# Performance work log

Hardware: AMD Instinct MI355X
Metric: run time of the kernel (lower is better)

## Reference

```python
import jax, jax.numpy as jnp
import numpy as np

N_AQI, N_MEO = 35, 18
N = N_AQI + N_MEO
F_OUT = 64
CTX = 60
D = F_OUT + CTX            # per-node feature dim inside pairwise concat
ALPHA = 0.2                # leakyrelu negative slope
B = 4096
IN_AQI, IN_MEO = 16, 16
NEG = -1e12


def _xavier(key, shape):
    fan_in, fan_out = shape[0], shape[-1]
    gain = 1.414
    bound = gain * np.sqrt(6.0 / (fan_in + fan_out))
    return jax.random.uniform(key, shape, jnp.float32, -bound, bound)


def setup_inputs() -> dict:
    key = jax.random.key(0)
    ks = jax.random.split(key, 32)
    inp = {
        "aqi_inp": jax.random.normal(ks[0], (B, N_AQI, IN_AQI), jnp.float32),
        "meo_inp": jax.random.normal(ks[1], (B, N_MEO, IN_MEO), jnp.float32),
        "context_feat": jax.random.normal(ks[2], (N, CTX), jnp.float32),
        "adj_norm": jax.random.uniform(ks[3], (N, N), jnp.float32),
        # embedding tables (all 2-dim embeddings as in the module)
        "aqi_idE": jax.random.normal(ks[4], (35, 2), jnp.float32),
        "aqi_monthE": jax.random.normal(ks[5], (13, 2), jnp.float32),
        "aqi_weekdayE": jax.random.normal(ks[6], (7, 2), jnp.float32),
        "aqi_hourE": jax.random.normal(ks[7], (24, 2), jnp.float32),
        "meo_windE": jax.random.normal(ks[8], (9, 2), jnp.float32),
        "meo_idE": jax.random.normal(ks[9], (18, 2), jnp.float32),
        "meo_monthE": jax.random.normal(ks[10], (13, 2), jnp.float32),
        "meo_weekdayE": jax.random.normal(ks[11], (7, 2), jnp.float32),
        "meo_hourE": jax.random.normal(ks[12], (24, 2), jnp.float32),
        # projection weights
        "W_xa": _xavier(ks[13], (IN_AQI, F_OUT)),
        "W_xm": _xavier(ks[14], (IN_MEO, F_OUT)),
        "W_ua": _xavier(ks[15], (IN_AQI + 8, F_OUT)),
        "W_um": _xavier(ks[16], (IN_MEO + 10, F_OUT)),
        # attention vectors: 2*F_OUT + 121 = 2*D + 1
        "a_aa": _xavier(ks[17], (2 * F_OUT + 121, 1)),
        "a_am": _xavier(ks[18], (2 * F_OUT + 121, 1)),
        "a_ma": _xavier(ks[19], (2 * F_OUT + 121, 1)),
        "a_mm": _xavier(ks[20], (2 * F_OUT + 121, 1)),
        # integer inputs
        "aqi_ex": jax.random.randint(ks[21], (B, N_AQI, 4), 0, 7, jnp.int32),
        "meo_ex": jax.random.randint(ks[22], (B, N_MEO, 5), 0, 7, jnp.int32),
        "adj": jax.random.randint(ks[23], (N, N), 0, 2, jnp.int32),
    }
    return inp


def _block(hf_src, hf_dst, an_block, a):
    # e[b,i,j] = leakyrelu(hf_src[b,i].a_src + hf_dst[b,j].a_dst + an[i,j]*a_last)
    d = hf_src.shape[-1]
    s = hf_src @ a[:d, 0]                        # [B, Ns]
    t = hf_dst @ a[d:2 * d, 0]                   # [B, Nd]
    e = s[:, :, None] + t[:, None, :] + an_block * a[2 * d, 0]
    return jax.nn.leaky_relu(e, ALPHA)


def reference(aqi_inp, meo_inp, context_feat, adj_norm,
              aqi_idE, aqi_monthE, aqi_weekdayE, aqi_hourE,
              meo_windE, meo_idE, meo_monthE, meo_weekdayE, meo_hourE,
              W_xa, W_xm, W_ua, W_um, a_aa, a_am, a_ma, a_mm,
              aqi_ex, meo_ex, adj):
    # value projection (pre-embedding features)
    attri_aqi = aqi_inp @ W_xa                   # [B, 35, F]
    attri_meo = meo_inp @ W_xm                   # [B, 18, F]
    heter_attri = jnp.concatenate([attri_aqi, attri_meo], axis=1)  # [B, 53, F]

    # append external-feature embeddings
    aqi_full = jnp.concatenate([
        aqi_inp, aqi_idE[aqi_ex[:, :, 0]], aqi_monthE[aqi_ex[:, :, 1]],
        aqi_weekdayE[aqi_ex[:, :, 2]], aqi_hourE[aqi_ex[:, :, 3]]], axis=2)
    meo_full = jnp.concatenate([
        meo_inp, meo_windE[meo_ex[:, :, 0]], meo_idE[meo_ex[:, :, 1]],
        meo_monthE[meo_ex[:, :, 2]], meo_weekdayE[meo_ex[:, :, 3]],
        meo_hourE[meo_ex[:, :, 4]]], axis=2)

    heter_aqi = aqi_full @ W_ua                  # [B, 35, F]
    heter_meo = meo_full @ W_um                  # [B, 18, F]
    hf = jnp.concatenate([heter_aqi, heter_meo], axis=1)            # [B, 53, F]
    ctx = jnp.broadcast_to(context_feat[None], (hf.shape[0], N, CTX))
    hf = jnp.concatenate([hf, ctx], axis=2)      # [B, 53, D]

    # pairwise scores per heterogeneous sub-block (decomposed, no N*N*D tensor)
    hfa, hfm = hf[:, :N_AQI], hf[:, N_AQI:]
    e_aa = _block(hfa, hfa, adj_norm[:N_AQI, :N_AQI], a_aa)
    e_am = _block(hfa, hfm, adj_norm[:N_AQI, N_AQI:], a_am)
    e_ma = _block(hfm, hfa, adj_norm[N_AQI:, :N_AQI], a_ma)
    e_mm = _block(hfm, hfm, adj_norm[N_AQI:, N_AQI:], a_mm)
    e = jnp.concatenate([
        jnp.concatenate([e_aa, e_am], axis=2),
        jnp.concatenate([e_ma, e_mm], axis=2)], axis=1)             # [B, 53, 53]

    attention = jax.nn.softmax(jnp.where(adj[None] > 0, e, NEG), axis=2)
    heter_out = attention @ heter_attri          # [B, 53, F]
    return heter_out[:, :N_AQI, :], heter_out[:, N_AQI:, :]
```

## Files before the change

### kernel.cpp

```cpp
#include <hip/hip_runtime.h>
#include <hip/hip_bf16.h>

#define NAQ 35
#define NME 18
#define NN  53
#define FD  64
#define CTXD 60
#define PERB 2

#define CVI_F   1024
#define CVE_F   1152
#define SVC_F   1248
#define EBW_F   1460
#define WS_FLOATS 4428

#define L_CVI   0
#define L_CVE   128
#define L_SVC   224
#define L_AF    436
#define L_EFA   1716
#define L_EFM   2031
#define L_SVW   2229
#define L_PT    2444
#define L_ATT   4748
#define S_TOTAL 7052
#define P_STR   72
#define AF_STR  40

typedef unsigned int   u32;
typedef unsigned short u16;
typedef short s8v __attribute__((ext_vector_type(8)));
typedef float f4v __attribute__((ext_vector_type(4)));

__device__ __forceinline__ float ldf(const void* p, long i, bool bf) {
  if (bf) { u16 h = ((const u16*)p)[i]; return __uint_as_float(((u32)h) << 16); }
  return ((const float*)p)[i];
}
__device__ __forceinline__ u16 f2bf(float f) {
  u32 u = __float_as_uint(f);
  return (u16)((u + 0x7FFFu + ((u >> 16) & 1u)) >> 16);
}
__device__ __forceinline__ bool sniff_bf16(const void* ctx) {
  const u32* w = (const u32*)ctx;
  bool ok = true;
#pragma unroll
  for (int k = 0; k < 32; ++k) {
    u32 e = (w[k] >> 7) & 0xFFu;
    ok = ok && (e >= 96u && e <= 160u);
  }
  return ok;
}
__device__ __forceinline__ s8v ld_frag(const u16* p) {
  union { float4 f; s8v s; } u;
  u.f = *(const float4*)(const void*)p;
  return u.s;
}

__global__ void prep_kernel(
    const void* __restrict__ ctx, const void* __restrict__ adjn,
    const void* __restrict__ Wxa, const void* __restrict__ Wxm,
    const void* __restrict__ Wua, const void* __restrict__ Wum,
    const void* __restrict__ a_aa, const void* __restrict__ a_am,
    const void* __restrict__ a_ma, const void* __restrict__ a_mm,
    const int* __restrict__ adj, float* __restrict__ ws)
{
  const bool bf = sniff_bf16(ctx);
  int tid = blockIdx.x * blockDim.x + threadIdx.x;
  if (tid < 2048) {
    int n = tid >> 5, kk = tid & 31;
    float v = (kk < 16) ? ldf(Wxa, kk * 64 + n, bf)
                        : ldf(Wxm, (kk - 16) * 64 + n, bf);
    ((u16*)ws)[tid] = f2bf(v);
    return;
  }
  int fi = tid - 1024;
  if (fi < CVE_F) {
    int idx = fi - CVI_F;
    int tr = idx >> 4, k = idx & 15;
    const void* Wu = (tr < 4) ? Wua : Wum;
    const void* av; int off;
    switch (tr) {
      case 0: av = a_aa; off = 0;   break;
      case 1: av = a_am; off = 0;   break;
      case 2: av = a_aa; off = 124; break;
      case 3: av = a_ma; off = 124; break;
      case 4: av = a_ma; off = 0;   break;
      case 5: av = a_mm; off = 0;   break;
      case 6: av = a_am; off = 124; break;
      default: av = a_mm; off = 124; break;
    }
    float s = 0.f;
    for (int f = 0; f < 64; ++f) s += ldf(Wu, k * 64 + f, bf) * ldf(av, off + f, bf);
    ws[fi] = s;
  } else if (fi < SVC_F) {
    int idx = fi - CVE_F;
    int tr = idx / 12, e = idx - tr * 12;
    int E = (tr < 4) ? 8 : 10;
    float v = 0.f;
    if (e < E) {
      const void* Wu = (tr < 4) ? Wua : Wum;
      const void* av; int off;
      switch (tr) {
        case 0: av = a_aa; off = 0;   break;
        case 1: av = a_am; off = 0;   break;
        case 2: av = a_aa; off = 124; break;
        case 3: av = a_ma; off = 124; break;
        case 4: av = a_ma; off = 0;   break;
        case 5: av = a_mm; off = 0;   break;
        case 6: av = a_am; off = 124; break;
        default: av = a_mm; off = 124; break;
      }
      float s = 0.f;
      for (int f = 0; f < 64; ++f) s += ldf(Wu, (16 + e) * 64 + f, bf) * ldf(av, off + f, bf);
      v = s;
    }
    ws[fi] = v;
  } else if (fi < EBW_F) {
    int idx = fi - SVC_F;
    int arr = idx / 53, i = idx - arr * 53;
    int isA = (i < NAQ);
    const void* av; int off;
    if (arr == 0)      { av = isA ? a_aa : a_ma; off = 64;  }
    else if (arr == 1) { av = isA ? a_am : a_mm; off = 64;  }
    else if (arr == 2) { av = isA ? a_aa : a_am; off = 188; }
    else               { av = isA ? a_ma : a_mm; off = 188; }
    float s = 0.f;
    for (int c = 0; c < CTXD; ++c) s += ldf(ctx, i * CTXD + c, bf) * ldf(av, off + c, bf);
    ws[fi] = s;
  } else if (fi < WS_FLOATS) {
    int idx = fi - EBW_F;
    int i = idx / 56, j = idx - i * 56;
    float v = 1e30f;
    if (j < NN && adj[i * NN + j] > 0) {
      const void* aq = (i < NAQ) ? ((j < NAQ) ? a_aa : a_am)
                                 : ((j < NAQ) ? a_ma : a_mm);
      v = ldf(adjn, i * NN + j, bf) * ldf(aq, 248, bf);
    }
    ws[fi] = v;
  }
}

__global__ __launch_bounds__(256, 5) void hga_main(
    const void* __restrict__ aqi_inp, const void* __restrict__ meo_inp,
    const void* __restrict__ ctx,
    const void* __restrict__ aqi_idE, const void* __restrict__ aqi_monthE,
    const void* __restrict__ aqi_weekdayE, const void* __restrict__ aqi_hourE,
    const void* __restrict__ meo_windE, const void* __restrict__ meo_idE,
    const void* __restrict__ meo_monthE, const void* __restrict__ meo_weekdayE,
    const void* __restrict__ meo_hourE,
    const int* __restrict__ aqi_ex, const int* __restrict__ meo_ex,
    const float* __restrict__ ws, void* __restrict__ out, int B)
{
  __shared__ __align__(16) float sm[S_TOTAL];
  const int t = threadIdx.x;
  const bool bf = sniff_bf16(ctx);
  u16* AFu = (u16*)(sm + L_AF);
  u16* ATu = (u16*)(sm + L_ATT);
  u16* Pu  = (u16*)(sm + L_PT);

  {
    const float4* src = (const float4*)(ws + CVI_F);
    float4* dst = (float4*)sm;
    for (int v = t; v < 109; v += 256) dst[v] = src[v];
  }
  __syncthreads();

  for (int e = 0; e < PERB; ++e) {
    const int b = blockIdx.x * PERB + e;
    if (b >= B) break;

    for (int idx = t; idx < 654; idx += 256) {
      if (idx < 140) {
        int r = idx >> 2, j = idx & 3;
        uint2 v;
        if (bf) v = ((const uint2*)aqi_inp)[((long)b * NAQ + r) * 4 + j];
        else {
          float4 f = ((const float4*)aqi_inp)[((long)b * NAQ + r) * 4 + j];
          v.x = ((u32)f2bf(f.y) << 16) | f2bf(f.x);
          v.y = ((u32)f2bf(f.w) << 16) | f2bf(f.z);
        }
        *(uint2*)(AFu + r * AF_STR + j * 4) = v;
      } else if (idx < 212) {
        int z = idx - 140;
        int i = z >> 2, j = z & 3;
        uint2 v;
        if (bf) v = ((const uint2*)meo_inp)[((long)b * NME + i) * 4 + j];
        else {
          float4 f = ((const float4*)meo_inp)[((long)b * NME + i) * 4 + j];
          v.x = ((u32)f2bf(f.y) << 16) | f2bf(f.x);
          v.y = ((u32)f2bf(f.w) << 16) | f2bf(f.z);
        }
        *(uint2*)(AFu + (NAQ + i) * AF_STR + 16 + j * 4) = v;
      } else if (idx < 352) {
        int z = idx - 212;
        int r = z >> 2, j = z & 3;
        *(uint2*)(AFu + r * AF_STR + 16 + j * 4) = make_uint2(0, 0);
      } else if (idx < 424) {
        int z = idx - 352;
        int i = z >> 2, j = z & 3;
        *(uint2*)(AFu + (NAQ + i) * AF_STR + j * 4) = make_uint2(0, 0);
      } else if (idx < 564) {
        int z = idx - 424;
        int r = z >> 2, p = z & 3;
        int ee = aqi_ex[((long)b * NAQ + r) * 4 + p];
        const void* tbl = (p == 0) ? aqi_idE : (p == 1) ? aqi_monthE
                         : (p == 2) ? aqi_weekdayE : aqi_hourE;
        sm[L_EFA + r * 9 + p * 2]     = ldf(tbl, ee * 2, bf);
        sm[L_EFA + r * 9 + p * 2 + 1] = ldf(tbl, ee * 2 + 1, bf);
      } else {
        int z = idx - 564;
        int i = z / 5, p = z - i * 5;
        int ee = meo_ex[((long)b * NME + i) * 5 + p];
        const void* tbl = (p == 0) ? meo_windE : (p == 1) ? meo_idE
                         : (p == 2) ? meo_monthE : (p == 3) ? meo_weekdayE : meo_hourE;
        sm[L_EFM + i * 11 + p * 2]     = ldf(tbl, ee * 2, bf);
        sm[L_EFM + i * 11 + p * 2 + 1] = ldf(tbl, ee * 2 + 1, bf);
      }
    }
    {
      int c = t & 63;
      for (int kk = t >> 6; kk < 11; kk += 4) ATu[c * P_STR + 53 + kk] = 0;
    }
    __syncthreads();

    {
      const int lane = t & 63, w = t >> 6;
      const int mm = lane & 15, q4 = lane >> 4;
      s8v av = ld_frag(AFu + (16 * w + mm) * AF_STR + q4 * 8);
      const u16* wt = (const u16*)ws;
      s8v bv0 = ld_frag(wt + (mm)      * 32 + q4 * 8);
      s8v bv1 = ld_frag(wt + (16 + mm) * 32 + q4 * 8);
      s8v bv2 = ld_frag(wt + (32 + mm) * 32 + q4 * 8);
      s8v bv3 = ld_frag(wt + (48 + mm) * 32 + q4 * 8);
#pragma unroll
      for (int nt = 0; nt < 4; ++nt) {
        f4v acc = {0.f, 0.f, 0.f, 0.f};
        s8v bv = (nt == 0) ? bv0 : (nt == 1) ? bv1 : (nt == 2) ? bv2 : bv3;
        acc = __builtin_amdgcn_mfma_f32_16x16x32_bf16(av, bv, acc, 0, 0, 0);
        const int c = nt * 16 + mm;
#pragma unroll
        for (int reg = 0; reg < 4; ++reg) {
          const int r = 16 * w + q4 * 4 + reg;
          if (r < NN) ATu[c * P_STR + r] = f2bf(acc[reg]);
        }
      }
      if (t < 212) {
        const int r = t >> 2, role = t & 3;
        const bool isA = (r < NAQ);
        const int tr = (isA ? 0 : 4) + role;
        const u16* arow = AFu + r * AF_STR + (isA ? 0 : 16);
        const float* Ci = sm + L_CVI + tr * 16;
        float s = 0.f;
#pragma unroll
        for (int k = 0; k < 16; ++k)
          s = fmaf(__uint_as_float(((u32)arow[k]) << 16), Ci[k], s);
        const int E = isA ? 8 : 10;
        const float* Ef = isA ? (sm + L_EFA + r * 9) : (sm + L_EFM + (r - NAQ) * 11);
        const float* Ce = sm + L_CVE + tr * 12;
        for (int k = 0; k < E; ++k) s = fmaf(Ef[k], Ce[k], s);
        sm[L_SVW + role * 53 + r] = sm[L_SVC + role * 53 + r] + s;
      }
    }
    __syncthreads();

    {
      const int r = t >> 2, q = t & 3;
      const int j0 = q * 14;
      if (r < NN) {
        float ev[14];
        float m = -3.0e38f, ssum = 0.f;
        const float s1 = sm[L_SVW + r], s2 = sm[L_SVW + 53 + r];
        const float* tb = sm + L_SVW + ((r < NAQ) ? 106 : 159);
        const float* ebrow = ws + EBW_F + r * 56;
#pragma unroll
        for (int jj = 0; jj < 14; ++jj) {
          const int j = j0 + jj;
          float v = -3.0e38f;
          if (j < NN) {
            float eb = ebrow[j];
            float rr = ((j < NAQ) ? s1 : s2) + tb[j] + eb;
            v = (eb > 1e29f) ? -1.0e12f : ((rr > 0.f) ? rr : 0.2f * rr);
          }
          ev[jj] = v;
          m = fmaxf(m, v);
        }
        m = fmaxf(m, __shfl_xor(m, 1, 64));
        m = fmaxf(m, __shfl_xor(m, 2, 64));
#pragma unroll
        for (int jj = 0; jj < 14; ++jj) {
          float pv = ((j0 + jj) < NN) ? __expf(ev[jj] - m) : 0.f;
          ev[jj] = pv;
          ssum += pv;
        }
        ssum += __shfl_xor(ssum, 1, 64);
        ssum += __shfl_xor(ssum, 2, 64);
        const float rinv = 1.f / ssum;
#pragma unroll
        for (int jj = 0; jj < 14; ++jj) {
          const int j = j0 + jj;
          Pu[r * P_STR + j] = (j < NN) ? f2bf(ev[jj] * rinv) : (u16)0;
        }
        if (q == 0) *(uint4*)(Pu + r * P_STR + 56) = make_uint4(0, 0, 0, 0);
      } else {
        for (int idx = t - 212; idx < 99; idx += 44) {
          int row = 53 + idx / 9, o = idx - (idx / 9) * 9;
          *(uint4*)(Pu + row * P_STR + o * 8) = make_uint4(0, 0, 0, 0);
        }
      }
    }
    __syncthreads();

    {
      const int lane = t & 63, w = t >> 6;
      const int mm = lane & 15, q4 = lane >> 4;
      const u16* Ar = Pu + (16 * w + mm) * P_STR + q4 * 8;
      s8v av0 = ld_frag(Ar);
      s8v av1 = ld_frag(Ar + 32);
#pragma unroll
      for (int nt = 0; nt < 4; ++nt) {
        const u16* Br = ATu + (16 * nt + mm) * P_STR + q4 * 8;
        s8v bv0 = ld_frag(Br);
        s8v bv1 = ld_frag(Br + 32);
        f4v acc = {0.f, 0.f, 0.f, 0.f};
        acc = __builtin_amdgcn_mfma_f32_16x16x32_bf16(av0, bv0, acc, 0, 0, 0);
        acc = __builtin_amdgcn_mfma_f32_16x16x32_bf16(av1, bv1, acc, 0, 0, 0);
        const int cgl = 16 * nt + mm;
#pragma unroll
        for (int reg = 0; reg < 4; ++reg) {
          const int rg = 16 * w + q4 * 4 + reg;
          if (rg < NN) {
            long off = (rg < NAQ)
              ? (long)b * (NAQ * FD) + (long)rg * FD + cgl
              : (long)B * (NAQ * FD) + (long)b * (NME * FD) + (long)(rg - NAQ) * FD + cgl;
            if (bf) ((u16*)out)[off] = f2bf(acc[reg]);
            else    ((float*)out)[off] = acc[reg];
          }
        }
      }
    }
    __syncthreads();
  }
}

extern "C" void kernel_launch(void* const* d_in, const int* in_sizes, int n_in,
                              void* d_out, int out_size, void* d_ws, size_t ws_size,
                              hipStream_t stream)
{
  const void* aqi_inp      = d_in[0];
  const void* meo_inp      = d_in[1];
  const void* ctx          = d_in[2];
  const void* adjn         = d_in[3];
  const void* aqi_idE      = d_in[4];
  const void* aqi_monthE   = d_in[5];
  const void* aqi_weekdayE = d_in[6];
  const void* aqi_hourE    = d_in[7];
  const void* meo_windE    = d_in[8];
  const void* meo_idE      = d_in[9];
  const void* meo_monthE   = d_in[10];
  const void* meo_weekdayE = d_in[11];
  const void* meo_hourE    = d_in[12];
  const void* Wxa          = d_in[13];
  const void* Wxm          = d_in[14];
  const void* Wua          = d_in[15];
  const void* Wum          = d_in[16];
  const void* a_aa         = d_in[17];
  const void* a_am         = d_in[18];
  const void* a_ma         = d_in[19];
  const void* a_mm         = d_in[20];
  const int*  aqi_ex       = (const int*)d_in[21];
  const int*  meo_ex       = (const int*)d_in[22];
  const int*  adj          = (const int*)d_in[23];
  float* ws = (float*)d_ws;
  const int B = in_sizes[0] / (NAQ * 16);

  hipLaunchKernelGGL(prep_kernel, dim3((5452 + 255) / 256), dim3(256), 0, stream,
                     ctx, adjn, Wxa, Wxm, Wua, Wum, a_aa, a_am, a_ma, a_mm, adj, ws);
  hipLaunchKernelGGL(hga_main, dim3((B + PERB - 1) / PERB), dim3(256), 0, stream,
                     aqi_inp, meo_inp, ctx, aqi_idE, aqi_monthE, aqi_weekdayE, aqi_hourE,
                     meo_windE, meo_idE, meo_monthE, meo_weekdayE, meo_hourE,
                     aqi_ex, meo_ex, ws, d_out, B);
}
```

Measured before the change: 177.4 us.

## Process one batch element per wave with register-resident MFMA attention pipeline

Restructures the main kernel so each of eight waves handles a whole batch element independently. Inputs and embeddings load straight into MFMA fragments, score projections run on MFMA with hi/lo bf16 splitting, softmax is done in registers, and the projected features are transposed via lane shuffles instead of shared memory. Per-element block barriers disappear. The prep kernel now folds the context terms into a precomputed per-pair bias, at the cost of more register pressure and extra MFMA work for the precision split.

```diff
diff --git a/kernel.cpp b/kernel.cpp
--- a/kernel.cpp
+++ b/kernel.cpp
@@ -1,37 +1,19 @@
 #include <hip/hip_runtime.h>
-#include <hip/hip_bf16.h>
 
 #define NAQ 35
 #define NME 18
 #define NN  53
 #define FD  64
 #define CTXD 60
-#define PERB 2
-
-#define CVI_F   1024
-#define CVE_F   1152
-#define SVC_F   1248
-#define EBW_F   1460
-#define WS_FLOATS 4428
-
-#define L_CVI   0
-#define L_CVE   128
-#define L_SVC   224
-#define L_AF    436
-#define L_EFA   1716
-#define L_EFM   2031
-#define L_SVW   2229
-#define L_PT    2444
-#define L_ATT   4748
-#define S_TOTAL 7052
-#define P_STR   72
-#define AF_STR  40
+#define WAVES 8
 
 typedef unsigned int   u32;
 typedef unsigned short u16;
 typedef short s8v __attribute__((ext_vector_type(8)));
 typedef float f4v __attribute__((ext_vector_type(4)));
 
+#define WS_EB_F 1280
+
 __device__ __forceinline__ float ldf(const void* p, long i, bool bf) {
   if (bf) { u16 h = ((const u16*)p)[i]; return __uint_as_float(((u32)h) << 16); }
   return ((const float*)p)[i];
@@ -40,6 +22,9 @@
   u32 u = __float_as_uint(f);
   return (u16)((u + 0x7FFFu + ((u >> 16) & 1u)) >> 16);
 }
+__device__ __forceinline__ float bf2f(u16 h) {
+  return __uint_as_float(((u32)h) << 16);
+}
 __device__ __forceinline__ bool sniff_bf16(const void* ctx) {
   const u32* w = (const u32*)ctx;
   bool ok = true;
@@ -50,10 +35,53 @@
   }
   return ok;
 }
-__device__ __forceinline__ s8v ld_frag(const u16* p) {
+__device__ __forceinline__ s8v ld_fragu(const u16* p) {
   union { float4 f; s8v s; } u;
   u.f = *(const float4*)(const void*)p;
   return u.s;
+}
+__device__ __forceinline__ s8v pack8f(float4 a, float4 b) {
+  union { u32 u[4]; s8v s; } U;
+  U.u[0] = (u32)f2bf(a.x) | ((u32)f2bf(a.y) << 16);
+  U.u[1] = (u32)f2bf(a.z) | ((u32)f2bf(a.w) << 16);
+  U.u[2] = (u32)f2bf(b.x) | ((u32)f2bf(b.y) << 16);
+  U.u[3] = (u32)f2bf(b.z) | ((u32)f2bf(b.w) << 16);
+  return U.s;
+}
+__device__ __forceinline__ s8v load_inp8(const void* p, long idx, bool bf) {
+  if (bf) {
+    union { uint4 u; s8v s; } U;
+    U.u = *(const uint4*)((const u16*)p + idx);
+    return U.s;
+  }
+  float4 f0 = *(const float4*)((const float*)p + idx);
+  float4 f1 = *(const float4*)((const float*)p + idx + 4);
+  return pack8f(f0, f1);
+}
+__device__ __forceinline__ void pack_hl(const float* e, s8v* hi, s8v* lo) {
+  union { u32 u[4]; s8v s; } H, L;
+#pragma unroll
+  for (int w = 0; w < 4; ++w) {
+    u16 h0 = f2bf(e[2*w]), h1 = f2bf(e[2*w+1]);
+    float l0 = e[2*w] - bf2f(h0), l1 = e[2*w+1] - bf2f(h1);
+    H.u[w] = (u32)h0 | ((u32)h1 << 16);
+    L.u[w] = (u32)f2bf(l0) | ((u32)f2bf(l1) << 16);
+  }
+  *hi = H.s; *lo = L.s;
+}
+__device__ __forceinline__ void avsel(int tr,
+    const void* a_aa, const void* a_am, const void* a_ma, const void* a_mm,
+    const void** av, int* off) {
+  switch (tr) {
+    case 0: *av = a_aa; *off = 0;   break;
+    case 1: *av = a_am; *off = 0;   break;
+    case 2: *av = a_aa; *off = 124; break;
+    case 3: *av = a_ma; *off = 124; break;
+    case 4: *av = a_ma; *off = 0;   break;
+    case 5: *av = a_mm; *off = 0;   break;
+    case 6: *av = a_am; *off = 124; break;
+    default:*av = a_mm; *off = 124; break;
+  }
 }
 
 __global__ void prep_kernel(
@@ -73,74 +101,48 @@
     ((u16*)ws)[tid] = f2bf(v);
     return;
   }
-  int fi = tid - 1024;
-  if (fi < CVE_F) {
-    int idx = fi - CVI_F;
-    int tr = idx >> 4, k = idx & 15;
-    const void* Wu = (tr < 4) ? Wua : Wum;
-    const void* av; int off;
-    switch (tr) {
-      case 0: av = a_aa; off = 0;   break;
-      case 1: av = a_am; off = 0;   break;
-      case 2: av = a_aa; off = 124; break;
-      case 3: av = a_ma; off = 124; break;
-      case 4: av = a_ma; off = 0;   break;
-      case 5: av = a_mm; off = 0;   break;
-      case 6: av = a_am; off = 124; break;
-      default: av = a_mm; off = 124; break;
-    }
-    float s = 0.f;
-    for (int f = 0; f < 64; ++f) s += ldf(Wu, k * 64 + f, bf) * ldf(av, off + f, bf);
-    ws[fi] = s;
-  } else if (fi < SVC_F) {
-    int idx = fi - CVE_F;
-    int tr = idx / 12, e = idx - tr * 12;
-    int E = (tr < 4) ? 8 : 10;
-    float v = 0.f;
-    if (e < E) {
-      const void* Wu = (tr < 4) ? Wua : Wum;
+  if (tid < 2560) {
+    int idx = tid - 2048;
+    int half = idx >> 8, rem = idx & 255;
+    int role = rem >> 6, k = rem & 63;
+    float w = 0.f;
+    const void* Wu = nullptr; int kk = -1, tr = 0;
+    if (k < 16)      { Wu = Wua; kk = k;           tr = role;     }
+    else if (k < 32) { Wu = Wum; kk = k - 16;      tr = 4 + role; }
+    else if (k < 40) { Wu = Wua; kk = 16 + (k-32); tr = role;     }
+    else if (k < 50) { Wu = Wum; kk = 16 + (k-40); tr = 4 + role; }
+    if (kk >= 0) {
       const void* av; int off;
-      switch (tr) {
-        case 0: av = a_aa; off = 0;   break;
-        case 1: av = a_am; off = 0;   break;
-        case 2: av = a_aa; off = 124; break;
-        case 3: av = a_ma; off = 124; break;
-        case 4: av = a_ma; off = 0;   break;
-        case 5: av = a_mm; off = 0;   break;
-        case 6: av = a_am; off = 124; break;
-        default: av = a_mm; off = 124; break;
+      avsel(tr, a_aa, a_am, a_ma, a_mm, &av, &off);
+      float s = 0.f;
+      for (int f = 0; f < 64; ++f) s += ldf(Wu, kk * 64 + f, bf) * ldf(av, off + f, bf);
+      w = s;
+    }
+    u16 hi = f2bf(w);
+    u16 val = hi;
+    if (half) { float lo = w - bf2f(hi); val = f2bf(lo); }
+    ((u16*)ws)[2048 + idx] = val;
+    return;
+  }
+  if (tid < 5952) {
+    int e = tid - 2560;
+    int r = e >> 6, j = e & 63;
+    float v = 1e30f;
+    if (j < NN && adj[r * NN + j] > 0) {
+      const void* aq = (r < NAQ) ? ((j < NAQ) ? a_aa : a_am)
+                                 : ((j < NAQ) ? a_ma : a_mm);
+      float s = ldf(adjn, r * NN + j, bf) * ldf(aq, 248, bf);
+      for (int c = 0; c < CTXD; ++c) {
+        s += ldf(ctx, r * CTXD + c, bf) * ldf(aq, 64 + c, bf);
+        s += ldf(ctx, j * CTXD + c, bf) * ldf(aq, 188 + c, bf);
       }
-      float s = 0.f;
-      for (int f = 0; f < 64; ++f) s += ldf(Wu, (16 + e) * 64 + f, bf) * ldf(av, off + f, bf);
       v = s;
     }
-    ws[fi] = v;
-  } else if (fi < EBW_F) {
-    int idx = fi - SVC_F;
-    int arr = idx / 53, i = idx - arr * 53;
-    int isA = (i < NAQ);
-    const void* av; int off;
-    if (arr == 0)      { av = isA ? a_aa : a_ma; off = 64;  }
-    else if (arr == 1) { av = isA ? a_am : a_mm; off = 64;  }
-    else if (arr == 2) { av = isA ? a_aa : a_am; off = 188; }
-    else               { av = isA ? a_ma : a_mm; off = 188; }
-    float s = 0.f;
-    for (int c = 0; c < CTXD; ++c) s += ldf(ctx, i * CTXD + c, bf) * ldf(av, off + c, bf);
-    ws[fi] = s;
-  } else if (fi < WS_FLOATS) {
-    int idx = fi - EBW_F;
-    int i = idx / 56, j = idx - i * 56;
-    float v = 1e30f;
-    if (j < NN && adj[i * NN + j] > 0) {
-      const void* aq = (i < NAQ) ? ((j < NAQ) ? a_aa : a_am)
-                                 : ((j < NAQ) ? a_ma : a_mm);
-      v = ldf(adjn, i * NN + j, bf) * ldf(aq, 248, bf);
-    }
-    ws[fi] = v;
-  }
-}
-
-__global__ __launch_bounds__(256, 5) void hga_main(
+    ws[WS_EB_F + e] = v;
+  }
+}
+
+__global__ __launch_bounds__(512, 4) void hga_main(
     const void* __restrict__ aqi_inp, const void* __restrict__ meo_inp,
     const void* __restrict__ ctx,
     const void* __restrict__ aqi_idE, const void* __restrict__ aqi_monthE,
@@ -151,194 +153,216 @@
     const int* __restrict__ aqi_ex, const int* __restrict__ meo_ex,
     const float* __restrict__ ws, void* __restrict__ out, int B)
 {
-  __shared__ __align__(16) float sm[S_TOTAL];
+  __shared__ __align__(16) u16  sWtA[64 * 40];
+  __shared__ __align__(16) u16  sWtPhi[16 * 72];
+  __shared__ __align__(16) u16  sWtPlo[16 * 72];
+  __shared__ __align__(16) float sEB[64 * 68];
+  __shared__ __align__(16) float sSVW[WAVES * 256];
+
   const int t = threadIdx.x;
   const bool bf = sniff_bf16(ctx);
-  u16* AFu = (u16*)(sm + L_AF);
-  u16* ATu = (u16*)(sm + L_ATT);
-  u16* Pu  = (u16*)(sm + L_PT);
-
-  {
-    const float4* src = (const float4*)(ws + CVI_F);
-    float4* dst = (float4*)sm;
-    for (int v = t; v < 109; v += 256) dst[v] = src[v];
+
+  for (int u = t; u < 256; u += 512) {
+    int row = u >> 2, c = u & 3;
+    *(uint4*)(sWtA + row * 40 + c * 8) = ((const uint4*)ws)[u];
+  }
+  for (int u = t; u < 256; u += 512) {
+    int half = u >> 7, u2 = u & 127;
+    int row = u2 >> 3, c = u2 & 7;
+    uint4 v = make_uint4(0, 0, 0, 0);
+    if (row < 4) v = ((const uint4*)ws)[256 + half * 32 + row * 8 + c];
+    u16* dst = half ? sWtPlo : sWtPhi;
+    *(uint4*)(dst + row * 72 + c * 8) = v;
+  }
+  for (int u = t; u < 1024; u += 512) {
+    int r = u >> 4, f = u & 15;
+    float4 v4 = make_float4(1e30f, 1e30f, 1e30f, 1e30f);
+    if (r < NN) v4 = *(const float4*)(ws + WS_EB_F + r * 64 + f * 4);
+    *(float4*)(sEB + r * 68 + f * 4) = v4;
   }
   __syncthreads();
 
-  for (int e = 0; e < PERB; ++e) {
-    const int b = blockIdx.x * PERB + e;
-    if (b >= B) break;
-
-    for (int idx = t; idx < 654; idx += 256) {
-      if (idx < 140) {
-        int r = idx >> 2, j = idx & 3;
-        uint2 v;
-        if (bf) v = ((const uint2*)aqi_inp)[((long)b * NAQ + r) * 4 + j];
-        else {
-          float4 f = ((const float4*)aqi_inp)[((long)b * NAQ + r) * 4 + j];
-          v.x = ((u32)f2bf(f.y) << 16) | f2bf(f.x);
-          v.y = ((u32)f2bf(f.w) << 16) | f2bf(f.z);
+  const int wv = t >> 6, lane = t & 63;
+  const int mm = lane & 15, q4 = lane >> 4;
+  const int b = blockIdx.x * WAVES + wv;
+  if (b >= B) return;
+
+  s8v av0[4], a1h[4], a1l[4];
+  const s8v zero8 = {0, 0, 0, 0, 0, 0, 0, 0};
+#pragma unroll
+  for (int i = 0; i < 4; ++i) {
+    const int r = 16 * i + mm;
+    s8v v0 = zero8, vh = zero8, vl = zero8;
+    if (r < NN) {
+      if (r < NAQ) {
+        if (q4 < 2) v0 = load_inp8(aqi_inp, ((long)b * NAQ + r) * 16 + q4 * 8, bf);
+        if (q4 == 0) {
+          const int4 ix = *(const int4*)(aqi_ex + ((long)b * NAQ + r) * 4);
+          float e[8];
+          e[0] = ldf(aqi_idE,      ix.x * 2, bf);  e[1] = ldf(aqi_idE,      ix.x * 2 + 1, bf);
+          e[2] = ldf(aqi_monthE,   ix.y * 2, bf);  e[3] = ldf(aqi_monthE,   ix.y * 2 + 1, bf);
+          e[4] = ldf(aqi_weekdayE, ix.z * 2, bf);  e[5] = ldf(aqi_weekdayE, ix.z * 2 + 1, bf);
+          e[6] = ldf(aqi_hourE,    ix.w * 2, bf);  e[7] = ldf(aqi_hourE,    ix.w * 2 + 1, bf);
+          pack_hl(e, &vh, &vl);
         }
-        *(uint2*)(AFu + r * AF_STR + j * 4) = v;
-      } else if (idx < 212) {
-        int z = idx - 140;
-        int i = z >> 2, j = z & 3;
-        uint2 v;
-        if (bf) v = ((const uint2*)meo_inp)[((long)b * NME + i) * 4 + j];
-        else {
-          float4 f = ((const float4*)meo_inp)[((long)b * NME + i) * 4 + j];
-          v.x = ((u32)f2bf(f.y) << 16) | f2bf(f.x);
-          v.y = ((u32)f2bf(f.w) << 16) | f2bf(f.z);
-        }
-        *(uint2*)(AFu + (NAQ + i) * AF_STR + 16 + j * 4) = v;
-      } else if (idx < 352) {
-        int z = idx - 212;
-        int r = z >> 2, j = z & 3;
-        *(uint2*)(AFu + r * AF_STR + 16 + j * 4) = make_uint2(0, 0);
-      } else if (idx < 424) {
-        int z = idx - 352;
-        int i = z >> 2, j = z & 3;
-        *(uint2*)(AFu + (NAQ + i) * AF_STR + j * 4) = make_uint2(0, 0);
-      } else if (idx < 564) {
-        int z = idx - 424;
-        int r = z >> 2, p = z & 3;
-        int ee = aqi_ex[((long)b * NAQ + r) * 4 + p];
-        const void* tbl = (p == 0) ? aqi_idE : (p == 1) ? aqi_monthE
-                         : (p == 2) ? aqi_weekdayE : aqi_hourE;
-        sm[L_EFA + r * 9 + p * 2]     = ldf(tbl, ee * 2, bf);
-        sm[L_EFA + r * 9 + p * 2 + 1] = ldf(tbl, ee * 2 + 1, bf);
       } else {
-        int z = idx - 564;
-        int i = z / 5, p = z - i * 5;
-        int ee = meo_ex[((long)b * NME + i) * 5 + p];
-        const void* tbl = (p == 0) ? meo_windE : (p == 1) ? meo_idE
-                         : (p == 2) ? meo_monthE : (p == 3) ? meo_weekdayE : meo_hourE;
-        sm[L_EFM + i * 11 + p * 2]     = ldf(tbl, ee * 2, bf);
-        sm[L_EFM + i * 11 + p * 2 + 1] = ldf(tbl, ee * 2 + 1, bf);
-      }
-    }
-    {
-      int c = t & 63;
-      for (int kk = t >> 6; kk < 11; kk += 4) ATu[c * P_STR + 53 + kk] = 0;
-    }
-    __syncthreads();
-
-    {
-      const int lane = t & 63, w = t >> 6;
-      const int mm = lane & 15, q4 = lane >> 4;
-      s8v av = ld_frag(AFu + (16 * w + mm) * AF_STR + q4 * 8);
-      const u16* wt = (const u16*)ws;
-      s8v bv0 = ld_frag(wt + (mm)      * 32 + q4 * 8);
-      s8v bv1 = ld_frag(wt + (16 + mm) * 32 + q4 * 8);
-      s8v bv2 = ld_frag(wt + (32 + mm) * 32 + q4 * 8);
-      s8v bv3 = ld_frag(wt + (48 + mm) * 32 + q4 * 8);
-#pragma unroll
-      for (int nt = 0; nt < 4; ++nt) {
-        f4v acc = {0.f, 0.f, 0.f, 0.f};
-        s8v bv = (nt == 0) ? bv0 : (nt == 1) ? bv1 : (nt == 2) ? bv2 : bv3;
-        acc = __builtin_amdgcn_mfma_f32_16x16x32_bf16(av, bv, acc, 0, 0, 0);
-        const int c = nt * 16 + mm;
-#pragma unroll
-        for (int reg = 0; reg < 4; ++reg) {
-          const int r = 16 * w + q4 * 4 + reg;
-          if (r < NN) ATu[c * P_STR + r] = f2bf(acc[reg]);
+        const int ri = r - NAQ;
+        if (q4 >= 2) v0 = load_inp8(meo_inp, ((long)b * NME + ri) * 16 + (q4 - 2) * 8, bf);
+        if (q4 == 1) {
+          const int* ix = meo_ex + ((long)b * NME + ri) * 5;
+          float e[8];
+          e[0] = ldf(meo_windE,    ix[0] * 2, bf); e[1] = ldf(meo_windE,    ix[0] * 2 + 1, bf);
+          e[2] = ldf(meo_idE,      ix[1] * 2, bf); e[3] = ldf(meo_idE,      ix[1] * 2 + 1, bf);
+          e[4] = ldf(meo_monthE,   ix[2] * 2, bf); e[5] = ldf(meo_monthE,   ix[2] * 2 + 1, bf);
+          e[6] = ldf(meo_weekdayE, ix[3] * 2, bf); e[7] = ldf(meo_weekdayE, ix[3] * 2 + 1, bf);
+          pack_hl(e, &vh, &vl);
+        } else if (q4 == 2) {
+          int i4 = meo_ex[((long)b * NME + ri) * 5 + 4];
+          float e[8] = {0.f, 0.f, 0.f, 0.f, 0.f, 0.f, 0.f, 0.f};
+          e[0] = ldf(meo_hourE, i4 * 2, bf);  e[1] = ldf(meo_hourE, i4 * 2 + 1, bf);
+          pack_hl(e, &vh, &vl);
         }
       }
-      if (t < 212) {
-        const int r = t >> 2, role = t & 3;
-        const bool isA = (r < NAQ);
-        const int tr = (isA ? 0 : 4) + role;
-        const u16* arow = AFu + r * AF_STR + (isA ? 0 : 16);
-        const float* Ci = sm + L_CVI + tr * 16;
-        float s = 0.f;
-#pragma unroll
-        for (int k = 0; k < 16; ++k)
-          s = fmaf(__uint_as_float(((u32)arow[k]) << 16), Ci[k], s);
-        const int E = isA ? 8 : 10;
-        const float* Ef = isA ? (sm + L_EFA + r * 9) : (sm + L_EFM + (r - NAQ) * 11);
-        const float* Ce = sm + L_CVE + tr * 12;
-        for (int k = 0; k < E; ++k) s = fmaf(Ef[k], Ce[k], s);
-        sm[L_SVW + role * 53 + r] = sm[L_SVC + role * 53 + r] + s;
+    }
+    av0[i] = v0; a1h[i] = vh; a1l[i] = vl;
+  }
+
+  s8v bh0 = ld_fragu(sWtPhi + mm * 72 + q4 * 8);
+  s8v bh1 = ld_fragu(sWtPhi + mm * 72 + (4 + q4) * 8);
+  s8v bl0 = ld_fragu(sWtPlo + mm * 72 + q4 * 8);
+  s8v bl1 = ld_fragu(sWtPlo + mm * 72 + (4 + q4) * 8);
+  f4v pacc[4];
+#pragma unroll
+  for (int i = 0; i < 4; ++i) {
+    f4v a = {0.f, 0.f, 0.f, 0.f};
+    a = __builtin_amdgcn_mfma_f32_16x16x32_bf16(av0[i], bh0, a, 0, 0, 0);
+    a = __builtin_amdgcn_mfma_f32_16x16x32_bf16(av0[i], bl0, a, 0, 0, 0);
+    a = __builtin_amdgcn_mfma_f32_16x16x32_bf16(a1h[i], bh1, a, 0, 0, 0);
+    a = __builtin_amdgcn_mfma_f32_16x16x32_bf16(a1h[i], bl1, a, 0, 0, 0);
+    if (!bf)
+      a = __builtin_amdgcn_mfma_f32_16x16x32_bf16(a1l[i], bh1, a, 0, 0, 0);
+    pacc[i] = a;
+  }
+  if (mm < 4) {
+    float* wbase = sSVW + wv * 256 + ((mm >= 2) ? 128 : 0) + (mm & 1);
+#pragma unroll
+    for (int i = 0; i < 4; ++i)
+#pragma unroll
+      for (int reg = 0; reg < 4; ++reg) {
+        int row = 16 * i + q4 * 4 + reg;
+        wbase[row * 2] = pacc[i][reg];
       }
-    }
-    __syncthreads();
-
-    {
-      const int r = t >> 2, q = t & 3;
-      const int j0 = q * 14;
-      if (r < NN) {
-        float ev[14];
-        float m = -3.0e38f, ssum = 0.f;
-        const float s1 = sm[L_SVW + r], s2 = sm[L_SVW + 53 + r];
-        const float* tb = sm + L_SVW + ((r < NAQ) ? 106 : 159);
-        const float* ebrow = ws + EBW_F + r * 56;
-#pragma unroll
-        for (int jj = 0; jj < 14; ++jj) {
-          const int j = j0 + jj;
-          float v = -3.0e38f;
-          if (j < NN) {
-            float eb = ebrow[j];
-            float rr = ((j < NAQ) ? s1 : s2) + tb[j] + eb;
-            v = (eb > 1e29f) ? -1.0e12f : ((rr > 0.f) ? rr : 0.2f * rr);
-          }
-          ev[jj] = v;
-          m = fmaxf(m, v);
-        }
-        m = fmaxf(m, __shfl_xor(m, 1, 64));
-        m = fmaxf(m, __shfl_xor(m, 2, 64));
-#pragma unroll
-        for (int jj = 0; jj < 14; ++jj) {
-          float pv = ((j0 + jj) < NN) ? __expf(ev[jj] - m) : 0.f;
-          ev[jj] = pv;
-          ssum += pv;
-        }
-        ssum += __shfl_xor(ssum, 1, 64);
-        ssum += __shfl_xor(ssum, 2, 64);
-        const float rinv = 1.f / ssum;
-#pragma unroll
-        for (int jj = 0; jj < 14; ++jj) {
-          const int j = j0 + jj;
-          Pu[r * P_STR + j] = (j < NN) ? f2bf(ev[jj] * rinv) : (u16)0;
-        }
-        if (q == 0) *(uint4*)(Pu + r * P_STR + 56) = make_uint4(0, 0, 0, 0);
-      } else {
-        for (int idx = t - 212; idx < 99; idx += 44) {
-          int row = 53 + idx / 9, o = idx - (idx / 9) * 9;
-          *(uint4*)(Pu + row * P_STR + o * 8) = make_uint4(0, 0, 0, 0);
+  }
+  asm volatile("s_waitcnt lgkmcnt(0)" ::: "memory");
+  __builtin_amdgcn_sched_barrier(0);
+
+  const float* sv = sSVW + wv * 256;
+  float2 tt[16];
+#pragma unroll
+  for (int c = 0; c < 8; ++c) {
+    tt[c]     = *(const float2*)(sv + 128 + (q4 * 8 + c) * 2);
+    tt[8 + c] = *(const float2*)(sv + 128 + (32 + q4 * 8 + c) * 2);
+  }
+  u32 paw[4][8];
+#pragma unroll
+  for (int i = 0; i < 4; ++i) {
+    const int r = 16 * i + mm;
+    float2 sp = *(const float2*)(sv + r * 2);
+    const float* ebr = sEB + r * 68;
+    float4 ea = *(const float4*)(ebr + q4 * 8);
+    float4 eb_ = *(const float4*)(ebr + q4 * 8 + 4);
+    float4 ec = *(const float4*)(ebr + 32 + q4 * 8);
+    float4 ed = *(const float4*)(ebr + 32 + q4 * 8 + 4);
+    float ebv[16] = {ea.x, ea.y, ea.z, ea.w, eb_.x, eb_.y, eb_.z, eb_.w,
+                     ec.x, ec.y, ec.z, ec.w, ed.x, ed.y, ed.z, ed.w};
+    const bool rA = (r < NAQ);
+    float v[16];
+    float m = -3.0e38f;
+#pragma unroll
+    for (int c = 0; c < 16; ++c) {
+      const int j = (c < 8) ? (q4 * 8 + c) : (32 + q4 * 8 + (c - 8));
+      float s = (j < NAQ) ? sp.x : sp.y;
+      float tv = rA ? tt[c].x : tt[c].y;
+      float x = s + tv + ebv[c];
+      float lk = fmaxf(x, 0.2f * x);
+      float val = (ebv[c] > 1e29f) ? -1.0e12f : lk;
+      v[c] = val;
+      m = fmaxf(m, val);
+    }
+    m = fmaxf(m, __shfl_xor(m, 16));
+    m = fmaxf(m, __shfl_xor(m, 32));
+    float sum = 0.f;
+#pragma unroll
+    for (int c = 0; c < 16; ++c) { float p = __expf(v[c] - m); v[c] = p; sum += p; }
+    sum += __shfl_xor(sum, 16);
+    sum += __shfl_xor(sum, 32);
+    const float rinv = 1.f / sum;
+#pragma unroll
+    for (int w = 0; w < 8; ++w) {
+      const int c0 = (w >> 2) * 8 + (w & 3) * 2;
+      paw[i][w] = (u32)f2bf(v[c0] * rinv) | ((u32)f2bf(v[c0 + 1] * rinv) << 16);
+    }
+  }
+
+  u32 rowoff[4][4];
+#pragma unroll
+  for (int i = 0; i < 4; ++i)
+#pragma unroll
+    for (int reg = 0; reg < 4; ++reg) {
+      int r = 16 * i + q4 * 4 + reg;
+      u32 off;
+      if (r < NAQ) off = ((u32)b * NAQ + (u32)r) * 64u + (u32)mm;
+      else off = (u32)B * (NAQ * 64u) + ((u32)b * NME + (u32)(r - NAQ)) * 64u + (u32)mm;
+      rowoff[i][reg] = off;
+    }
+
+  const int srcA = (2 * (q4 & 1)) * 16 + mm;
+  const int srcB = srcA + 16;
+  const bool hs = (q4 >= 2);
+#pragma unroll
+  for (int nt = 0; nt < 4; ++nt) {
+    s8v bw = ld_fragu(sWtA + (16 * nt + mm) * 40 + q4 * 8);
+    f4v ag[4];
+#pragma unroll
+    for (int i = 0; i < 4; ++i) {
+      f4v z = {0.f, 0.f, 0.f, 0.f};
+      ag[i] = __builtin_amdgcn_mfma_f32_16x16x32_bf16(av0[i], bw, z, 0, 0, 0);
+    }
+    u32 p0[4], p1[4];
+#pragma unroll
+    for (int i = 0; i < 4; ++i) {
+      p0[i] = (u32)f2bf(ag[i][0]) | ((u32)f2bf(ag[i][1]) << 16);
+      p1[i] = (u32)f2bf(ag[i][2]) | ((u32)f2bf(ag[i][3]) << 16);
+    }
+    union { u32 u[4]; s8v s; } W0, W1;
+    u32 x0, x1;
+    x0 = (u32)__shfl((int)p0[0], srcA); x1 = (u32)__shfl((int)p0[1], srcA); W0.u[0] = hs ? x1 : x0;
+    x0 = (u32)__shfl((int)p1[0], srcA); x1 = (u32)__shfl((int)p1[1], srcA); W0.u[1] = hs ? x1 : x0;
+    x0 = (u32)__shfl((int)p0[0], srcB); x1 = (u32)__shfl((int)p0[1], srcB); W0.u[2] = hs ? x1 : x0;
+    x0 = (u32)__shfl((int)p1[0], srcB); x1 = (u32)__shfl((int)p1[1], srcB); W0.u[3] = hs ? x1 : x0;
+    x0 = (u32)__shfl((int)p0[2], srcA); x1 = (u32)__shfl((int)p0[3], srcA); W1.u[0] = hs ? x1 : x0;
+    x0 = (u32)__shfl((int)p1[2], srcA); x1 = (u32)__shfl((int)p1[3], srcA); W1.u[1] = hs ? x1 : x0;
+    x0 = (u32)__shfl((int)p0[2], srcB); x1 = (u32)__shfl((int)p0[3], srcB); W1.u[2] = hs ? x1 : x0;
+    x0 = (u32)__shfl((int)p1[2], srcB); x1 = (u32)__shfl((int)p1[3], srcB); W1.u[3] = hs ? x1 : x0;
+    s8v bt0 = W0.s, bt1 = W1.s;
+#pragma unroll
+    for (int i = 0; i < 4; ++i) {
+      union { u32 u[4]; s8v s; } A0, A1;
+      A0.u[0] = paw[i][0]; A0.u[1] = paw[i][1]; A0.u[2] = paw[i][2]; A0.u[3] = paw[i][3];
+      A1.u[0] = paw[i][4]; A1.u[1] = paw[i][5]; A1.u[2] = paw[i][6]; A1.u[3] = paw[i][7];
+      f4v acc = {0.f, 0.f, 0.f, 0.f};
+      acc = __builtin_amdgcn_mfma_f32_16x16x32_bf16(A0.s, bt0, acc, 0, 0, 0);
+      acc = __builtin_amdgcn_mfma_f32_16x16x32_bf16(A1.s, bt1, acc, 0, 0, 0);
+#pragma unroll
+      for (int reg = 0; reg < 4; ++reg) {
+        int r = 16 * i + q4 * 4 + reg;
+        if (r < NN) {
+          u32 off = rowoff[i][reg] + 16u * (u32)nt;
+          if (bf) ((u16*)out)[off] = f2bf(acc[reg]);
+          else    ((float*)out)[off] = acc[reg];
         }
       }
     }
-    __syncthreads();
-
-    {
-      const int lane = t & 63, w = t >> 6;
-      const int mm = lane & 15, q4 = lane >> 4;
-      const u16* Ar = Pu + (16 * w + mm) * P_STR + q4 * 8;
-      s8v av0 = ld_frag(Ar);
-      s8v av1 = ld_frag(Ar + 32);
-#pragma unroll
-      for (int nt = 0; nt < 4; ++nt) {
-        const u16* Br = ATu + (16 * nt + mm) * P_STR + q4 * 8;
-        s8v bv0 = ld_frag(Br);
-        s8v bv1 = ld_frag(Br + 32);
-        f4v acc = {0.f, 0.f, 0.f, 0.f};
-        acc = __builtin_amdgcn_mfma_f32_16x16x32_bf16(av0, bv0, acc, 0, 0, 0);
-        acc = __builtin_amdgcn_mfma_f32_16x16x32_bf16(av1, bv1, acc, 0, 0, 0);
-        const int cgl = 16 * nt + mm;
-#pragma unroll
-        for (int reg = 0; reg < 4; ++reg) {
-          const int rg = 16 * w + q4 * 4 + reg;
-          if (rg < NN) {
-            long off = (rg < NAQ)
-              ? (long)b * (NAQ * FD) + (long)rg * FD + cgl
-              : (long)B * (NAQ * FD) + (long)b * (NME * FD) + (long)(rg - NAQ) * FD + cgl;
-            if (bf) ((u16*)out)[off] = f2bf(acc[reg]);
-            else    ((float*)out)[off] = acc[reg];
-          }
-        }
-      }
-    }
-    __syncthreads();
   }
 }
 
@@ -369,13 +393,13 @@
   const void* a_mm         = d_in[20];
   const int*  aqi_ex       = (const int*)d_in[21];
   const int*  meo_ex       = (const int*)d_in[22];
-  const int*  adj          = (const int*)d_in[23];
   float* ws = (float*)d_ws;
   const int B = in_sizes[0] / (NAQ * 16);
 
-  hipLaunchKernelGGL(prep_kernel, dim3((5452 + 255) / 256), dim3(256), 0, stream,
-                     ctx, adjn, Wxa, Wxm, Wua, Wum, a_aa, a_am, a_ma, a_mm, adj, ws);
-  hipLaunchKernelGGL(hga_main, dim3((B + PERB - 1) / PERB), dim3(256), 0, stream,
+  hipLaunchKernelGGL(prep_kernel, dim3((5952 + 255) / 256), dim3(256), 0, stream,
+                     ctx, adjn, Wxa, Wxm, Wua, Wum, a_aa, a_am, a_ma, a_mm,
+                     (const int*)d_in[23], ws);
+  hipLaunchKernelGGL(hga_main, dim3((B + WAVES - 1) / WAVES), dim3(512), 0, stream,
                      aqi_inp, meo_inp, ctx, aqi_idE, aqi_monthE, aqi_weekdayE, aqi_hourE,
                      meo_windE, meo_idE, meo_monthE, meo_weekdayE, meo_hourE,
                      aqi_ex, meo_ex, ws, d_out, B);
```

Result: faster. 162.2 us (-8.5%).
